# Kernel tuning notes

Measured on AMD Instinct MI355X. Metric: run time of the kernel, lower is better.

The kernel has to match this reference:

```python
import jax, jax.numpy as jnp
import numpy as np

H = 32        # query heads
KVH = 8       # key/value heads (GQA)
D = 160       # head_dim = 5120 / 32
ROT = 40      # rotary_ndims = head_dim * partial_rotary_factor (0.25)
THETA = 10000.0
NEG = -1e30


def setup_inputs() -> dict:
    key = jax.random.key(0)
    k0, k1, k2, k3 = jax.random.split(key, 4)
    B, S, E = 1, 2048, 5120
    QKV_OUT = H * D + 2 * KVH * D  # 7680
    hidden_states = jax.random.normal(k0, (B, S, E), jnp.float32)
    w_qkv = jax.random.normal(k1, (QKV_OUT, E), jnp.float32) * 0.02
    b_qkv = jax.random.normal(k2, (QKV_OUT,), jnp.float32) * 0.02
    w_o = jax.random.normal(k3, (E, E), jnp.float32) * 0.02
    positions = jnp.arange(S, dtype=jnp.int32)
    return {"hidden_states": hidden_states, "positions": positions,
            "w_qkv": w_qkv, "b_qkv": b_qkv, "w_o": w_o}


def _partial_rope(x, cos, sin):
    # x: [B,S,h,D]; neox-style rotation on first ROT dims, pass-through rest
    rot, rest = x[..., :ROT], x[..., ROT:]
    x1, x2 = jnp.split(rot, 2, axis=-1)
    rotated = jnp.concatenate([x1 * cos - x2 * sin, x2 * cos + x1 * sin], axis=-1)
    return jnp.concatenate([rotated, rest], axis=-1)


def reference(hidden_states, positions, w_qkv, b_qkv, w_o):
    B, S, E = hidden_states.shape
    qkv = jnp.einsum('bse,oe->bso', hidden_states, w_qkv) + b_qkv
    q = qkv[..., :H * D].reshape(B, S, H, D)
    k = qkv[..., H * D:H * D + KVH * D].reshape(B, S, KVH, D)
    v = qkv[..., H * D + KVH * D:].reshape(B, S, KVH, D)

    # partial rotary embedding
    inv_freq = 1.0 / (THETA ** (jnp.arange(0, ROT, 2, dtype=jnp.float32) / ROT))
    freqs = positions.astype(jnp.float32)[:, None] * inv_freq  # [S, ROT/2]
    cos = jnp.cos(freqs)[None, :, None, :]
    sin = jnp.sin(freqs)[None, :, None, :]
    q = _partial_rope(q, cos, sin)
    k = _partial_rope(k, cos, sin)

    # grouped-query causal attention (prefill path of PagedAttention)
    G = H // KVH
    qg = q.reshape(B, S, KVH, G, D)
    scores = jnp.einsum('bqkgd,bskd->bkgqs', qg, k) * (D ** -0.5)
    causal = jnp.tril(jnp.ones((S, S), bool))
    scores = jnp.where(causal, scores, NEG)
    attn = jax.nn.softmax(scores, axis=-1)
    out = jnp.einsum('bkgqs,bskd->bqkgd', attn, v).reshape(B, S, H * D)
    return jnp.einsum('bsf,ef->bse', out, w_o)
```

## Files before the change

### kernel.cpp

```cpp
#include <hip/hip_runtime.h>

typedef __attribute__((ext_vector_type(8))) short short8;
typedef __attribute__((ext_vector_type(4))) float f32x4;
typedef __attribute__((ext_vector_type(16))) float f32x16;
typedef __attribute__((ext_vector_type(4))) unsigned short ushort4v;
typedef __attribute__((ext_vector_type(4))) unsigned u32x4;

#define S_LEN 2048
#define E_DIM 5120
#define NH 32
#define NKVH 8
#define HD 160
#define QKV_OUT (NH*HD + 2*NKVH*HD)
#define NPAIR 20
#define ROT_D 40

__device__ __forceinline__ unsigned short f2b(float f) {
  unsigned u = __builtin_bit_cast(unsigned, f);
  u += 0x7fffu + ((u >> 16) & 1u);
  return (unsigned short)(u >> 16);
}
__device__ __forceinline__ float b2f(unsigned short b) {
  return __builtin_bit_cast(float, ((unsigned)b) << 16);
}

typedef const __attribute__((address_space(1))) unsigned gu32;
typedef __attribute__((address_space(3))) unsigned lu32;
__device__ __forceinline__ void gll16(const void* g, void* l) {
  __builtin_amdgcn_global_load_lds((gu32*)g, (lu32*)l, 16, 0, 0);
}
#define MFMA16(a, b, c) __builtin_amdgcn_mfma_f32_16x16x32_bf16(a, b, c, 0, 0, 0)
#define MFMA32(a, b, c) __builtin_amdgcn_mfma_f32_32x32x16_bf16(a, b, c, 0, 0, 0)
#define SBAR() asm volatile("s_barrier" ::: "memory")

__global__ __launch_bounds__(256) void f32_to_bf16_vec(const float* __restrict__ in,
                                                       unsigned short* __restrict__ out,
                                                       long n4) {
  long i = (long)blockIdx.x * blockDim.x + threadIdx.x;
  long stride = (long)gridDim.x * blockDim.x;
  for (; i < n4; i += stride) {
    float4 v = ((const float4*)in)[i];
    ushort4v o = { f2b(v.x), f2b(v.y), f2b(v.z), f2b(v.w) };
    ((ushort4v*)out)[i] = o;
  }
}

__global__ __launch_bounds__(256) void build_trig(const int* __restrict__ positions,
                                                  float* __restrict__ cosT,
                                                  float* __restrict__ sinT) {
  int idx = blockIdx.x * blockDim.x + threadIdx.x;
  if (idx >= S_LEN * NPAIR) return;
  int s = idx / NPAIR, i = idx - s * NPAIR;
  float inv = powf(10000.0f, -(float)i / (float)NPAIR);
  float f = (float)positions[s] * inv;
  cosT[idx] = cosf(f);
  sinT[idx] = sinf(f);
}

template <bool BIAS, bool OUT_BF16>
__global__ __launch_bounds__(512, 2) void gemm8(const unsigned short* __restrict__ A,
                                                const unsigned short* __restrict__ B,
                                                const float* __restrict__ bias,
                                                void* __restrict__ Cp,
                                                int N) {
  constexpr int K = E_DIM;
  constexpr int NT = K / 64;
  int bid = blockIdx.x;
  int bm = bid & 7, bn = bid >> 3;
  int tid = threadIdx.x;
  int w = tid >> 6, l = tid & 63;
  int g = l >> 4, c = l & 15;
  int wm = w >> 2, wn = w & 3;

  __shared__ __align__(16) unsigned short LA[2][2][8192];
  __shared__ __align__(16) unsigned short LB[2][2][8192];

  f32x4 acc[8][4];
#pragma unroll
  for (int i = 0; i < 8; ++i)
#pragma unroll
    for (int j = 0; j < 4; ++j) acc[i][j] = f32x4{0.f, 0.f, 0.f, 0.f};

  int uU[2] = {tid, 512 + tid};
  const unsigned short* Ag[2];
  const unsigned short* Bg[2];
#pragma unroll
  for (int j = 0; j < 2; ++j) {
    int u = uU[j];
    int wmG = u >> 9, rlA = (u >> 3) & 63, sl = u & 7;
    Ag[j] = A + (size_t)(bm * 256 + wmG * 128 + rlA) * K + (sl ^ (rlA & 7)) * 8;
    int wnG = u >> 8, rlB = (u >> 3) & 31;
    Bg[j] = B + (size_t)(bn * 256 + wnG * 64 + rlB) * K + (sl ^ (rlB & 7)) * 8;
  }

  auto stageA = [&](int t, int rg, int db) {
#pragma unroll
    for (int j = 0; j < 2; ++j)
      gll16(Ag[j] + (size_t)rg * 64 * K + t * 64, (char*)&LA[db][rg][0] + uU[j] * 16);
  };
  auto stageB = [&](int t, int cg, int db) {
#pragma unroll
    for (int j = 0; j < 2; ++j)
      gll16(Bg[j] + (size_t)cg * 32 * K + t * 64, (char*)&LB[db][cg][0] + uU[j] * 16);
  };

  int aA = wm * 4096 + c * 64;
  int bB = wn * 2048 + c * 64;
  int s0 = (g ^ (c & 7)) * 8;
  int s1 = ((4 + g) ^ (c & 7)) * 8;

  short8 a[8], b0[4], b1[4];

  stageA(0, 0, 0); stageB(0, 0, 0); stageB(0, 1, 0); stageA(0, 1, 0);
  stageA(1, 0, 1); stageB(1, 0, 1); stageB(1, 1, 1);
  asm volatile("s_waitcnt vmcnt(6)" ::: "memory");
  SBAR();

  for (int t = 0; t < NT; ++t) {
    int db = t & 1;
    const unsigned short* la0 = &LA[db][0][0];
    const unsigned short* la1 = &LA[db][1][0];
    const unsigned short* lb0 = &LB[db][0][0];
    const unsigned short* lb1 = &LB[db][1][0];
    bool tail = (t >= NT - 3);

#pragma unroll
    for (int fm = 0; fm < 4; ++fm) {
      a[2 * fm + 0] = *(const short8*)&la0[aA + fm * 1024 + s0];
      a[2 * fm + 1] = *(const short8*)&la0[aA + fm * 1024 + s1];
    }
#pragma unroll
    for (int fn = 0; fn < 2; ++fn) {
      b0[2 * fn + 0] = *(const short8*)&lb0[bB + fn * 1024 + s0];
      b0[2 * fn + 1] = *(const short8*)&lb0[bB + fn * 1024 + s1];
    }
    if (t + 1 < NT) stageA(t + 1, 1, db ^ 1);
    SBAR();
    __builtin_amdgcn_s_setprio(1);
#pragma unroll
    for (int fm = 0; fm < 4; ++fm)
#pragma unroll
      for (int fn = 0; fn < 2; ++fn) {
        acc[fm][fn] = MFMA16(a[2 * fm + 0], b0[2 * fn + 0], acc[fm][fn]);
        acc[fm][fn] = MFMA16(a[2 * fm + 1], b0[2 * fn + 1], acc[fm][fn]);
      }
    __builtin_amdgcn_s_setprio(0);
    SBAR();

#pragma unroll
    for (int fn = 0; fn < 2; ++fn) {
      b1[2 * fn + 0] = *(const short8*)&lb1[bB + fn * 1024 + s0];
      b1[2 * fn + 1] = *(const short8*)&lb1[bB + fn * 1024 + s1];
    }
    if (t + 2 < NT) stageA(t + 2, 0, db);
    SBAR();
    __builtin_amdgcn_s_setprio(1);
#pragma unroll
    for (int fm = 0; fm < 4; ++fm)
#pragma unroll
      for (int fn = 0; fn < 2; ++fn) {
        acc[fm][fn + 2] = MFMA16(a[2 * fm + 0], b1[2 * fn + 0], acc[fm][fn + 2]);
        acc[fm][fn + 2] = MFMA16(a[2 * fm + 1], b1[2 * fn + 1], acc[fm][fn + 2]);
      }
    __builtin_amdgcn_s_setprio(0);
    if (tail)
      asm volatile("s_waitcnt vmcnt(0)" ::: "memory");
    else
      asm volatile("s_waitcnt vmcnt(10)" ::: "memory");
    SBAR();

#pragma unroll
    for (int fm = 0; fm < 4; ++fm) {
      a[2 * fm + 0] = *(const short8*)&la1[aA + fm * 1024 + s0];
      a[2 * fm + 1] = *(const short8*)&la1[aA + fm * 1024 + s1];
    }
    if (t + 2 < NT) stageB(t + 2, 0, db);
    SBAR();
    __builtin_amdgcn_s_setprio(1);
#pragma unroll
    for (int fm = 0; fm < 4; ++fm)
#pragma unroll
      for (int fn = 0; fn < 2; ++fn) {
        acc[fm + 4][fn + 2] = MFMA16(a[2 * fm + 0], b1[2 * fn + 0], acc[fm + 4][fn + 2]);
        acc[fm + 4][fn + 2] = MFMA16(a[2 * fm + 1], b1[2 * fn + 1], acc[fm + 4][fn + 2]);
      }
    __builtin_amdgcn_s_setprio(0);
    SBAR();

    if (t + 2 < NT) stageB(t + 2, 1, db);
    SBAR();
    __builtin_amdgcn_s_setprio(1);
#pragma unroll
    for (int fm = 0; fm < 4; ++fm)
#pragma unroll
      for (int fn = 0; fn < 2; ++fn) {
        acc[fm + 4][fn] = MFMA16(a[2 * fm + 0], b0[2 * fn + 0], acc[fm + 4][fn]);
        acc[fm + 4][fn] = MFMA16(a[2 * fm + 1], b0[2 * fn + 1], acc[fm + 4][fn]);
      }
    __builtin_amdgcn_s_setprio(0);
    if (tail)
      asm volatile("s_waitcnt vmcnt(0)" ::: "memory");
    else
      asm volatile("s_waitcnt vmcnt(8)" ::: "memory");
    SBAR();
  }

#pragma unroll
  for (int FN = 0; FN < 4; ++FN) {
    int n = bn * 256 + wn * 64 + (FN >> 1) * 32 + (FN & 1) * 16 + c;
    float bv = BIAS ? bias[n] : 0.f;
#pragma unroll
    for (int FM = 0; FM < 8; ++FM) {
#pragma unroll
      for (int r = 0; r < 4; ++r) {
        int m = bm * 256 + wm * 128 + (FM >> 2) * 64 + (FM & 3) * 16 + 4 * g + r;
        float v = acc[FM][FN][r] + bv;
        if (OUT_BF16)
          ((unsigned short*)Cp)[(size_t)m * N + n] = f2b(v);
        else
          ((float*)Cp)[(size_t)m * N + n] = v;
      }
    }
  }
}

__global__ __launch_bounds__(256) void rope_qk(const unsigned short* __restrict__ qkv,
                                               const float* __restrict__ cosT,
                                               const float* __restrict__ sinT,
                                               unsigned short* __restrict__ Q,
                                               unsigned short* __restrict__ K) {
  int s = blockIdx.x;
  int tid = threadIdx.x;
  const unsigned short* row = qkv + (size_t)s * QKV_OUT;
  const float* cs = cosT + s * NPAIR;
  const float* sn = sinT + s * NPAIR;
  for (int p = tid; p < 40 * NPAIR; p += 256) {
    int head = p / NPAIR, i = p - head * NPAIR;
    float x1 = b2f(row[head * HD + i]);
    float x2 = b2f(row[head * HD + i + NPAIR]);
    float o1 = x1 * cs[i] - x2 * sn[i];
    float o2 = x2 * cs[i] + x1 * sn[i];
    unsigned short* dst = (head < NH) ? (Q + ((size_t)head * S_LEN + s) * HD)
                                      : (K + ((size_t)(head - NH) * S_LEN + s) * HD);
    dst[i] = f2b(o1);
    dst[i + NPAIR] = f2b(o2);
  }
  for (int u = tid; u < 40 * 15; u += 256) {
    int head = u / 15;
    int d8 = ROT_D + (u - head * 15) * 8;
    short8 v = *(const short8*)(row + head * HD + d8);
    unsigned short* dst = (head < NH) ? (Q + ((size_t)head * S_LEN + s) * HD)
                                      : (K + ((size_t)(head - NH) * S_LEN + s) * HD);
    *(short8*)(dst + d8) = v;
  }
}

__global__ __launch_bounds__(256) void v_transpose(const unsigned short* __restrict__ qkv,
                                                   unsigned short* __restrict__ Vt) {
  int st = blockIdx.x;
  int kvh = blockIdx.y;
  int tid = threadIdx.x;
  __shared__ __align__(16) unsigned short T[64][168];
  const unsigned short* src = qkv + (size_t)(st * 64) * QKV_OUT + NH * HD + NKVH * HD + kvh * HD;
#pragma unroll
  for (int i = 0; i < 5; ++i) {
    int u = tid + i * 256;
    int r = u / 20, sl = u - r * 20;
    int4 val = *(const int4*)(src + (size_t)r * QKV_OUT + sl * 8);
    *(int4*)((char*)&T[r][0] + sl * 16) = val;
  }
  __syncthreads();
  unsigned short* dst = Vt + (size_t)kvh * HD * S_LEN + st * 64;
#pragma unroll
  for (int i = 0; i < 5; ++i) {
    int u = tid + i * 256;
    int d = u >> 3, sc = u & 7;
    unsigned short tmp[8];
#pragma unroll
    for (int j = 0; j < 8; ++j) tmp[j] = T[sc * 8 + j][d];
    *(int4*)(dst + (size_t)d * S_LEN + sc * 8) = *(const int4*)tmp;
  }
}

__global__ __launch_bounds__(256, 1) void attn_kernel(const unsigned short* __restrict__ Q,
                                                      const unsigned short* __restrict__ K,
                                                      const unsigned short* __restrict__ Vt,
                                                      unsigned short* __restrict__ Ao) {
  int bid = blockIdx.x;
  int kvh = bid & 7;
  int sidx = bid >> 3;
  int strip = (sidx < 32) ? (63 - sidx) : (sidx - 32);
  int nt = strip + 1;
  int qbase = strip * 32;
  int tid = threadIdx.x;
  int w = tid >> 6, l = tid & 63;
  int lo5 = l & 31, hi = l >> 5;
  int h = kvh * 4 + w;

  __shared__ __align__(16) unsigned short KL[2][10 * 512];
  __shared__ __align__(16) unsigned short VL[2][10 * 512];

  const unsigned short* kg = K + (size_t)kvh * S_LEN * HD;
  const unsigned short* vg = Vt + (size_t)kvh * HD * S_LEN;
  const unsigned short* qg = Q + ((size_t)h * S_LEN + qbase + lo5) * HD;

  short8 qf[10];
#pragma unroll
  for (int f = 0; f < 10; ++f) qf[f] = *(const short8*)(qg + f * 16 + hi * 8);

  auto STAGE = [&](int t, int buf) {
#pragma unroll
    for (int i = 0; i < 5; ++i) {
      int cc = w * 5 + i;
      if (cc < 10) {
        gll16(kg + ((size_t)(t * 32) + lo5) * HD + cc * 16 + hi * 8,
              (void*)&KL[buf][cc * 512]);
      } else {
        int m = cc - 10;
        int dblk = m >> 1, half = m & 1;
        gll16(vg + (size_t)(dblk * 32 + lo5) * S_LEN + t * 32 + half * 16 + hi * 8,
              (void*)&VL[buf][m * 512]);
      }
    }
  };

  const float sm_scale = 0.07905694150420949f;
  f32x16 acc[5];
#pragma unroll
  for (int d = 0; d < 5; ++d)
#pragma unroll
    for (int r = 0; r < 16; ++r) acc[d][r] = 0.f;
  float l_run = 0.f;

  STAGE(0, 0);
  if (nt > 1) STAGE(1, 1);

#pragma unroll 1
  for (int t = 0; t < nt; ++t) {
    int buf = t & 1;
    if (t + 1 < nt)
      asm volatile("s_waitcnt vmcnt(5)" ::: "memory");
    else
      asm volatile("s_waitcnt vmcnt(0)" ::: "memory");
    SBAR();

    f32x16 S;
#pragma unroll
    for (int r = 0; r < 16; ++r) S[r] = 0.f;
    __builtin_amdgcn_s_setprio(1);
#pragma unroll
    for (int f = 0; f < 10; ++f) {
      short8 kf = *(const short8*)&KL[buf][f * 512 + l * 8];
      S = MFMA32(kf, qf[f], S);
    }
    __builtin_amdgcn_s_setprio(0);

    float e[16];
    float rsum = 0.f;
    if (t == nt - 1) {
#pragma unroll
      for (int r = 0; r < 16; ++r) {
        int kvloc = (r & 3) + 8 * (r >> 2) + 4 * hi;
        float x = (kvloc <= lo5) ? S[r] * sm_scale : -1e30f;
        e[r] = __expf(x);
        rsum += e[r];
      }
    } else {
#pragma unroll
      for (int r = 0; r < 16; ++r) {
        e[r] = __expf(S[r] * sm_scale);
        rsum += e[r];
      }
    }
    rsum += __shfl_xor(rsum, 32);
    l_run += rsum;

    unsigned xp[8];
#pragma unroll
    for (int i = 0; i < 8; ++i)
      asm("v_cvt_pk_bf16_f32 %0, %1, %2" : "=v"(xp[i]) : "v"(e[2 * i]), "v"(e[2 * i + 1]));
    asm volatile("v_permlane32_swap_b32 %0, %1" : "+v"(xp[0]), "+v"(xp[2]));
    asm volatile("v_permlane32_swap_b32 %0, %1" : "+v"(xp[1]), "+v"(xp[3]));
    asm volatile("v_permlane32_swap_b32 %0, %1" : "+v"(xp[4]), "+v"(xp[6]));
    asm volatile("v_permlane32_swap_b32 %0, %1" : "+v"(xp[5]), "+v"(xp[7]));
    u32x4 w0 = {xp[0], xp[1], xp[2], xp[3]};
    u32x4 w1 = {xp[4], xp[5], xp[6], xp[7]};
    short8 pa0 = __builtin_bit_cast(short8, w0);
    short8 pa1 = __builtin_bit_cast(short8, w1);

    __builtin_amdgcn_s_setprio(1);
#pragma unroll
    for (int dblk = 0; dblk < 5; ++dblk) {
      short8 v0 = *(const short8*)&VL[buf][(2 * dblk + 0) * 512 + l * 8];
      short8 v1 = *(const short8*)&VL[buf][(2 * dblk + 1) * 512 + l * 8];
      acc[dblk] = MFMA32(pa0, v0, acc[dblk]);
      acc[dblk] = MFMA32(pa1, v1, acc[dblk]);
    }
    __builtin_amdgcn_s_setprio(0);
    SBAR();
    if (t + 2 < nt) STAGE(t + 2, buf);
  }

  float rinv = 1.f / l_run;
  float ri[16];
#pragma unroll
  for (int r = 0; r < 16; ++r) ri[r] = __shfl(rinv, (r & 3) + 8 * (r >> 2) + 4 * hi);
#pragma unroll
  for (int dblk = 0; dblk < 5; ++dblk)
#pragma unroll
    for (int r = 0; r < 16; ++r) {
      int q = (r & 3) + 8 * (r >> 2) + 4 * hi;
      Ao[(size_t)(qbase + q) * E_DIM + h * HD + dblk * 32 + lo5] = f2b(acc[dblk][r] * ri[r]);
    }
}

extern "C" void kernel_launch(void* const* d_in, const int* in_sizes, int n_in,
                              void* d_out, int out_size, void* d_ws, size_t ws_size,
                              hipStream_t stream) {
  const float* hidden = (const float*)d_in[0];
  const int* positions = (const int*)d_in[1];
  const float* w_qkv = (const float*)d_in[2];
  const float* b_qkv = (const float*)d_in[3];
  const float* w_o = (const float*)d_in[4];
  float* out = (float*)d_out;

  char* ws = (char*)d_ws;
  size_t off = 0;
  auto alloc = [&](size_t bytes) {
    void* p = ws + off;
    off += (bytes + 255) & ~(size_t)255;
    return p;
  };
  unsigned short* hB = (unsigned short*)alloc((size_t)S_LEN * E_DIM * 2);
  unsigned short* wqkvB = (unsigned short*)alloc((size_t)QKV_OUT * E_DIM * 2);
  unsigned short* woB = (unsigned short*)alloc((size_t)E_DIM * E_DIM * 2);
  unsigned short* qkvB = (unsigned short*)alloc((size_t)S_LEN * QKV_OUT * 2);
  unsigned short* Qb = (unsigned short*)alloc((size_t)NH * S_LEN * HD * 2);
  unsigned short* Kb = (unsigned short*)alloc((size_t)NKVH * S_LEN * HD * 2);
  unsigned short* Vtb = (unsigned short*)alloc((size_t)NKVH * HD * S_LEN * 2);
  float* cosT = (float*)alloc((size_t)S_LEN * NPAIR * 4);
  float* sinT = (float*)alloc((size_t)S_LEN * NPAIR * 4);
  if (off > ws_size) return;

  unsigned short* Ao = hB;

  f32_to_bf16_vec<<<2048, 256, 0, stream>>>(hidden, hB, (long)S_LEN * E_DIM / 4);
  f32_to_bf16_vec<<<2048, 256, 0, stream>>>(w_qkv, wqkvB, (long)QKV_OUT * E_DIM / 4);
  f32_to_bf16_vec<<<2048, 256, 0, stream>>>(w_o, woB, (long)E_DIM * E_DIM / 4);
  build_trig<<<(S_LEN * NPAIR + 255) / 256, 256, 0, stream>>>(positions, cosT, sinT);

  gemm8<true, true><<<dim3((QKV_OUT / 256) * 8), 512, 0, stream>>>(
      hB, wqkvB, b_qkv, qkvB, QKV_OUT);

  rope_qk<<<S_LEN, 256, 0, stream>>>(qkvB, cosT, sinT, Qb, Kb);
  v_transpose<<<dim3(S_LEN / 64, NKVH), 256, 0, stream>>>(qkvB, Vtb);

  attn_kernel<<<dim3(512), 256, 0, stream>>>(Qb, Kb, Vtb, Ao);

  gemm8<false, false><<<dim3((E_DIM / 256) * 8), 512, 0, stream>>>(
      Ao, woB, nullptr, out, E_DIM);
}
```

Before: 489.2 us.

## Fuse fp32-to-bf16 weight conversion into GEMM B-operand staging

Removes the separate conversion kernels for w_qkv and w_o. The GEMM now loads fp32 weight tiles into registers, packs them to bf16 with v_cvt_pk_bf16_f32 and writes them to LDS, restructuring the pipeline's wait counts and stage placement. This avoids an extra full read and write of both weight matrices, but the GEMM reads twice as many B bytes and spends VALU and register work on conversion inside the main loop. The epilogue row/column indexing is also changed to match a new fragment mapping.

```diff
diff --git a/kernel.cpp b/kernel.cpp
--- a/kernel.cpp
+++ b/kernel.cpp
@@ -59,7 +59,7 @@
 
 template <bool BIAS, bool OUT_BF16>
 __global__ __launch_bounds__(512, 2) void gemm8(const unsigned short* __restrict__ A,
-                                                const unsigned short* __restrict__ B,
+                                                const float* __restrict__ Bf32,
                                                 const float* __restrict__ bias,
                                                 void* __restrict__ Cp,
                                                 int N) {
@@ -83,25 +83,54 @@
 
   int uU[2] = {tid, 512 + tid};
   const unsigned short* Ag[2];
-  const unsigned short* Bg[2];
 #pragma unroll
   for (int j = 0; j < 2; ++j) {
     int u = uU[j];
     int wmG = u >> 9, rlA = (u >> 3) & 63, sl = u & 7;
     Ag[j] = A + (size_t)(bm * 256 + wmG * 128 + rlA) * K + (sl ^ (rlA & 7)) * 8;
-    int wnG = u >> 8, rlB = (u >> 3) & 31;
-    Bg[j] = B + (size_t)(bn * 256 + wnG * 64 + rlB) * K + (sl ^ (rlB & 7)) * 8;
-  }
-
+  }
   auto stageA = [&](int t, int rg, int db) {
 #pragma unroll
     for (int j = 0; j < 2; ++j)
       gll16(Ag[j] + (size_t)rg * 64 * K + t * 64, (char*)&LA[db][rg][0] + uU[j] * 16);
   };
-  auto stageB = [&](int t, int cg, int db) {
-#pragma unroll
-    for (int j = 0; j < 2; ++j)
-      gll16(Bg[j] + (size_t)cg * 32 * K + t * 64, (char*)&LB[db][cg][0] + uU[j] * 16);
+
+  const float* Bpj[2];
+  int wofB[2];
+#pragma unroll
+  for (int j = 0; j < 2; ++j) {
+    int r = w * 16 + j * 8 + (l >> 3);
+    int sg = ((l & 7) ^ (r & 7)) * 8;
+    wofB[j] = (r * 8 + (l & 7)) * 16;
+    int rowg = (r >> 5) * 64 + (r & 31);
+    Bpj[j] = Bf32 + (size_t)(bn * 256 + rowg) * K + sg;
+  }
+  const size_t cgstep = (size_t)32 * K;
+
+  float4 bst[2][2][2];
+  auto issueB = [&](int t) {
+#pragma unroll
+    for (int cg = 0; cg < 2; ++cg)
+#pragma unroll
+      for (int j = 0; j < 2; ++j) {
+        const float* p = Bpj[j] + cg * cgstep + (size_t)t * 64;
+        bst[cg][j][0] = *(const float4*)p;
+        bst[cg][j][1] = *(const float4*)(p + 4);
+      }
+  };
+  auto writeB = [&](int db) {
+#pragma unroll
+    for (int cg = 0; cg < 2; ++cg)
+#pragma unroll
+      for (int j = 0; j < 2; ++j) {
+        unsigned w0, w1, w2, w3;
+        asm("v_cvt_pk_bf16_f32 %0, %1, %2" : "=v"(w0) : "v"(bst[cg][j][0].x), "v"(bst[cg][j][0].y));
+        asm("v_cvt_pk_bf16_f32 %0, %1, %2" : "=v"(w1) : "v"(bst[cg][j][0].z), "v"(bst[cg][j][0].w));
+        asm("v_cvt_pk_bf16_f32 %0, %1, %2" : "=v"(w2) : "v"(bst[cg][j][1].x), "v"(bst[cg][j][1].y));
+        asm("v_cvt_pk_bf16_f32 %0, %1, %2" : "=v"(w3) : "v"(bst[cg][j][1].z), "v"(bst[cg][j][1].w));
+        u32x4 pk = {w0, w1, w2, w3};
+        *(u32x4*)((char*)&LB[db][cg][0] + wofB[j]) = pk;
+      }
   };
 
   int aA = wm * 4096 + c * 64;
@@ -111,9 +140,15 @@
 
   short8 a[8], b0[4], b1[4];
 
-  stageA(0, 0, 0); stageB(0, 0, 0); stageB(0, 1, 0); stageA(0, 1, 0);
-  stageA(1, 0, 1); stageB(1, 0, 1); stageB(1, 1, 1);
-  asm volatile("s_waitcnt vmcnt(6)" ::: "memory");
+  issueB(0);
+  stageA(0, 0, 0); stageA(0, 1, 0);
+  stageA(1, 0, 1); stageA(1, 1, 1);
+  asm volatile("s_waitcnt vmcnt(8)" ::: "memory");
+  writeB(0);
+  issueB(1);
+  asm volatile("s_waitcnt vmcnt(0)" ::: "memory");
+  writeB(1);
+  asm volatile("s_waitcnt lgkmcnt(0)" ::: "memory");
   SBAR();
 
   for (int t = 0; t < NT; ++t) {
@@ -122,7 +157,7 @@
     const unsigned short* la1 = &LA[db][1][0];
     const unsigned short* lb0 = &LB[db][0][0];
     const unsigned short* lb1 = &LB[db][1][0];
-    bool tail = (t >= NT - 3);
+    bool have2 = (t + 2 < NT);
 
 #pragma unroll
     for (int fm = 0; fm < 4; ++fm) {
@@ -134,7 +169,7 @@
       b0[2 * fn + 0] = *(const short8*)&lb0[bB + fn * 1024 + s0];
       b0[2 * fn + 1] = *(const short8*)&lb0[bB + fn * 1024 + s1];
     }
-    if (t + 1 < NT) stageA(t + 1, 1, db ^ 1);
+    if (have2) issueB(t + 2);
     SBAR();
     __builtin_amdgcn_s_setprio(1);
 #pragma unroll
@@ -152,7 +187,7 @@
       b1[2 * fn + 0] = *(const short8*)&lb1[bB + fn * 1024 + s0];
       b1[2 * fn + 1] = *(const short8*)&lb1[bB + fn * 1024 + s1];
     }
-    if (t + 2 < NT) stageA(t + 2, 0, db);
+    if (have2) stageA(t + 2, 0, db);
     SBAR();
     __builtin_amdgcn_s_setprio(1);
 #pragma unroll
@@ -163,10 +198,6 @@
         acc[fm][fn + 2] = MFMA16(a[2 * fm + 1], b1[2 * fn + 1], acc[fm][fn + 2]);
       }
     __builtin_amdgcn_s_setprio(0);
-    if (tail)
-      asm volatile("s_waitcnt vmcnt(0)" ::: "memory");
-    else
-      asm volatile("s_waitcnt vmcnt(10)" ::: "memory");
     SBAR();
 
 #pragma unroll
@@ -174,7 +205,12 @@
       a[2 * fm + 0] = *(const short8*)&la1[aA + fm * 1024 + s0];
       a[2 * fm + 1] = *(const short8*)&la1[aA + fm * 1024 + s1];
     }
-    if (t + 2 < NT) stageB(t + 2, 0, db);
+    if (have2) {
+      asm volatile("s_waitcnt vmcnt(2)" ::: "memory");
+      writeB(db);
+    } else {
+      asm volatile("s_waitcnt vmcnt(0)" ::: "memory");
+    }
     SBAR();
     __builtin_amdgcn_s_setprio(1);
 #pragma unroll
@@ -185,10 +221,10 @@
         acc[fm + 4][fn + 2] = MFMA16(a[2 * fm + 1], b1[2 * fn + 1], acc[fm + 4][fn + 2]);
       }
     __builtin_amdgcn_s_setprio(0);
-    SBAR();
-
-    if (t + 2 < NT) stageB(t + 2, 1, db);
-    SBAR();
+    asm volatile("s_waitcnt lgkmcnt(0)" ::: "memory");
+    SBAR();
+
+    if (have2) stageA(t + 2, 1, db);
     __builtin_amdgcn_s_setprio(1);
 #pragma unroll
     for (int fm = 0; fm < 4; ++fm)
@@ -198,23 +234,19 @@
         acc[fm + 4][fn] = MFMA16(a[2 * fm + 1], b0[2 * fn + 1], acc[fm + 4][fn]);
       }
     __builtin_amdgcn_s_setprio(0);
-    if (tail)
-      asm volatile("s_waitcnt vmcnt(0)" ::: "memory");
-    else
-      asm volatile("s_waitcnt vmcnt(8)" ::: "memory");
-    SBAR();
-  }
-
-#pragma unroll
-  for (int FN = 0; FN < 4; ++FN) {
-    int n = bn * 256 + wn * 64 + (FN >> 1) * 32 + (FN & 1) * 16 + c;
+    SBAR();
+  }
+
+#pragma unroll
+  for (int fn = 0; fn < 4; ++fn) {
+    int n = bn * 256 + wn * 64 + fn * 16 + c;
     float bv = BIAS ? bias[n] : 0.f;
 #pragma unroll
-    for (int FM = 0; FM < 8; ++FM) {
+    for (int fm = 0; fm < 8; ++fm) {
 #pragma unroll
       for (int r = 0; r < 4; ++r) {
-        int m = bm * 256 + wm * 128 + (FM >> 2) * 64 + (FM & 3) * 16 + 4 * g + r;
-        float v = acc[FM][FN][r] + bv;
+        int m = bm * 256 + wm * 128 + fm * 16 + 4 * g + r;
+        float v = acc[fm][fn][r] + bv;
         if (OUT_BF16)
           ((unsigned short*)Cp)[(size_t)m * N + n] = f2b(v);
         else
@@ -432,8 +464,6 @@
     return p;
   };
   unsigned short* hB = (unsigned short*)alloc((size_t)S_LEN * E_DIM * 2);
-  unsigned short* wqkvB = (unsigned short*)alloc((size_t)QKV_OUT * E_DIM * 2);
-  unsigned short* woB = (unsigned short*)alloc((size_t)E_DIM * E_DIM * 2);
   unsigned short* qkvB = (unsigned short*)alloc((size_t)S_LEN * QKV_OUT * 2);
   unsigned short* Qb = (unsigned short*)alloc((size_t)NH * S_LEN * HD * 2);
   unsigned short* Kb = (unsigned short*)alloc((size_t)NKVH * S_LEN * HD * 2);
@@ -445,12 +475,10 @@
   unsigned short* Ao = hB;
 
   f32_to_bf16_vec<<<2048, 256, 0, stream>>>(hidden, hB, (long)S_LEN * E_DIM / 4);
-  f32_to_bf16_vec<<<2048, 256, 0, stream>>>(w_qkv, wqkvB, (long)QKV_OUT * E_DIM / 4);
-  f32_to_bf16_vec<<<2048, 256, 0, stream>>>(w_o, woB, (long)E_DIM * E_DIM / 4);
   build_trig<<<(S_LEN * NPAIR + 255) / 256, 256, 0, stream>>>(positions, cosT, sinT);
 
   gemm8<true, true><<<dim3((QKV_OUT / 256) * 8), 512, 0, stream>>>(
-      hB, wqkvB, b_qkv, qkvB, QKV_OUT);
+      hB, w_qkv, b_qkv, qkvB, QKV_OUT);
 
   rope_qk<<<S_LEN, 256, 0, stream>>>(qkvB, cosT, sinT, Qb, Kb);
   v_transpose<<<dim3(S_LEN / 64, NKVH), 256, 0, stream>>>(qkvB, Vtb);
@@ -458,5 +486,5 @@
   attn_kernel<<<dim3(512), 256, 0, stream>>>(Qb, Kb, Vtb, Ao);
 
   gemm8<false, false><<<dim3((E_DIM / 256) * 8), 512, 0, stream>>>(
-      Ao, woB, nullptr, out, E_DIM);
-}
+      Ao, w_o, nullptr, out, E_DIM);
+}
```

Result: slower. 641.2 us (+31.1%).

## Add 256x160-tile output-projection GEMM to fill all CUs; drop one barrier

Applied to the files above, without the earlier changes.

Adds a specialized gemm160 kernel for the output projection. It uses 256x160 tiles, so the grid has 256 blocks instead of 160, aiming to occupy every CU on the device and reduce wave-quantization idle time. Its B-operand staging is split into three chunks spread across the k-loop phases, with per-wave vmcnt waits. The QKV GEMM also loses one workgroup barrier before its second MFMA phase, and its epilogue index arithmetic is simplified to an equivalent form. The per-wave waitcnt schedule and the removed barrier add race risk if the counts or ordering are wrong.

```diff
diff --git a/kernel.cpp b/kernel.cpp
--- a/kernel.cpp
+++ b/kernel.cpp
@@ -188,7 +188,6 @@
     SBAR();
 
     if (t + 2 < NT) stageB(t + 2, 1, db);
-    SBAR();
     __builtin_amdgcn_s_setprio(1);
 #pragma unroll
     for (int fm = 0; fm < 4; ++fm)
@@ -207,18 +206,175 @@
 
 #pragma unroll
   for (int FN = 0; FN < 4; ++FN) {
-    int n = bn * 256 + wn * 64 + (FN >> 1) * 32 + (FN & 1) * 16 + c;
+    int n = bn * 256 + wn * 64 + FN * 16 + c;
     float bv = BIAS ? bias[n] : 0.f;
 #pragma unroll
     for (int FM = 0; FM < 8; ++FM) {
 #pragma unroll
       for (int r = 0; r < 4; ++r) {
-        int m = bm * 256 + wm * 128 + (FM >> 2) * 64 + (FM & 3) * 16 + 4 * g + r;
+        int m = bm * 256 + wm * 128 + FM * 16 + 4 * g + r;
         float v = acc[FM][FN][r] + bv;
         if (OUT_BF16)
           ((unsigned short*)Cp)[(size_t)m * N + n] = f2b(v);
         else
           ((float*)Cp)[(size_t)m * N + n] = v;
+      }
+    }
+  }
+}
+
+__global__ __launch_bounds__(512, 2) void gemm160(const unsigned short* __restrict__ A,
+                                                  const unsigned short* __restrict__ B,
+                                                  float* __restrict__ C) {
+  constexpr int K = E_DIM;
+  constexpr int NT = K / 64;
+  int bid = blockIdx.x;
+  int bm = bid & 7, bn = bid >> 3;
+  int tid = threadIdx.x;
+  int w = tid >> 6, l = tid & 63;
+  int g = l >> 4, c = l & 15;
+  int wm = w >> 1, wn = w & 1;
+
+  __shared__ __align__(16) unsigned short LA[2][2][8192];
+  __shared__ __align__(16) unsigned short LB[2][20 * 512];
+
+  f32x4 acc[4][5];
+#pragma unroll
+  for (int i = 0; i < 4; ++i)
+#pragma unroll
+    for (int j = 0; j < 5; ++j) acc[i][j] = f32x4{0.f, 0.f, 0.f, 0.f};
+
+  int uU[2] = {tid, 512 + tid};
+  const unsigned short* Ag[2];
+#pragma unroll
+  for (int j = 0; j < 2; ++j) {
+    int u = uU[j];
+    int wmG = u >> 9, rlA = (u >> 3) & 63, sl = u & 7;
+    Ag[j] = A + (size_t)(bm * 256 + wmG * 128 + rlA) * K + (sl ^ (rlA & 7)) * 8;
+  }
+  auto stageA = [&](int t, int rg, int db) {
+#pragma unroll
+    for (int j = 0; j < 2; ++j)
+      gll16(Ag[j] + (size_t)rg * 64 * K + t * 64, (char*)&LA[db][rg][0] + uU[j] * 16);
+  };
+
+  int rowin = l >> 3, slb = l & 7;
+  int swz = (slb ^ rowin) * 8;
+  int chN01 = (w < 4) ? w : 6 + w;
+  int chN23 = (w < 4) ? 4 + w : 10 + w;
+  int chN4 = (w < 2) ? 8 + w : 16 + w;
+  const unsigned short* srcN01 = B + (size_t)(bn * 160 + chN01 * 8 + rowin) * K + swz;
+  const unsigned short* srcN23 = B + (size_t)(bn * 160 + chN23 * 8 + rowin) * K + swz;
+  const unsigned short* srcN4 = B + (size_t)(bn * 160 + ((w < 4) ? chN4 * 8 : 0) + rowin) * K + swz;
+  auto stB = [&](const unsigned short* src, int ch, int t, int db) {
+    gll16(src + t * 64, (char*)&LB[db][0] + ch * 1024 + l * 16);
+  };
+
+  int rgA = wm & 1;
+  int aA = ((wm >> 1) * 64 + c) * 64;
+  int bB = (wn * 80 + c) * 64;
+  int s0 = (g ^ (c & 7)) * 8;
+  int s1 = ((4 + g) ^ (c & 7)) * 8;
+
+  short8 a[8], b01[4], b23[4], bn4[2];
+
+  stageA(0, 0, 0); stageA(0, 1, 0);
+  stB(srcN01, chN01, 0, 0); stB(srcN23, chN23, 0, 0);
+  if (w < 4) stB(srcN4, chN4, 0, 0);
+  stageA(1, 0, 1); stageA(1, 1, 1);
+  stB(srcN01, chN01, 1, 1); stB(srcN23, chN23, 1, 1);
+  asm volatile("s_waitcnt vmcnt(0)" ::: "memory");
+  SBAR();
+
+  for (int t = 0; t < NT; ++t) {
+    int db = t & 1;
+    const unsigned short* la = &LA[db][rgA][0];
+    const unsigned short* lb = &LB[db][0];
+    bool tail = (t >= NT - 2);
+
+#pragma unroll
+    for (int fm = 0; fm < 4; ++fm) {
+      a[2 * fm + 0] = *(const short8*)&la[aA + fm * 1024 + s0];
+      a[2 * fm + 1] = *(const short8*)&la[aA + fm * 1024 + s1];
+    }
+#pragma unroll
+    for (int fn = 0; fn < 2; ++fn) {
+      b01[2 * fn + 0] = *(const short8*)&lb[bB + fn * 1024 + s0];
+      b01[2 * fn + 1] = *(const short8*)&lb[bB + fn * 1024 + s1];
+    }
+    if (t + 1 < NT && w < 4) stB(srcN4, chN4, t + 1, db ^ 1);
+    SBAR();
+    __builtin_amdgcn_s_setprio(1);
+#pragma unroll
+    for (int fm = 0; fm < 4; ++fm)
+#pragma unroll
+      for (int fn = 0; fn < 2; ++fn) {
+        acc[fm][fn] = MFMA16(a[2 * fm + 0], b01[2 * fn + 0], acc[fm][fn]);
+        acc[fm][fn] = MFMA16(a[2 * fm + 1], b01[2 * fn + 1], acc[fm][fn]);
+      }
+    __builtin_amdgcn_s_setprio(0);
+    if (tail)
+      asm volatile("s_waitcnt vmcnt(0)" ::: "memory");
+    else if (w < 4)
+      asm volatile("s_waitcnt vmcnt(8)" ::: "memory");
+    else
+      asm volatile("s_waitcnt vmcnt(6)" ::: "memory");
+    SBAR();
+
+#pragma unroll
+    for (int fn = 0; fn < 2; ++fn) {
+      b23[2 * fn + 0] = *(const short8*)&lb[bB + (2 + fn) * 1024 + s0];
+      b23[2 * fn + 1] = *(const short8*)&lb[bB + (2 + fn) * 1024 + s1];
+    }
+    if (t + 2 < NT) {
+      stageA(t + 2, 0, db); stageA(t + 2, 1, db);
+      stB(srcN01, chN01, t + 2, db);
+    }
+    SBAR();
+    __builtin_amdgcn_s_setprio(1);
+#pragma unroll
+    for (int fm = 0; fm < 4; ++fm)
+#pragma unroll
+      for (int fn = 0; fn < 2; ++fn) {
+        acc[fm][fn + 2] = MFMA16(a[2 * fm + 0], b23[2 * fn + 0], acc[fm][fn + 2]);
+        acc[fm][fn + 2] = MFMA16(a[2 * fm + 1], b23[2 * fn + 1], acc[fm][fn + 2]);
+      }
+    __builtin_amdgcn_s_setprio(0);
+    if (tail)
+      asm volatile("s_waitcnt vmcnt(0)" ::: "memory");
+    else if (w < 4)
+      asm volatile("s_waitcnt vmcnt(12)" ::: "memory");
+    SBAR();
+
+    bn4[0] = *(const short8*)&lb[bB + 4 * 1024 + s0];
+    bn4[1] = *(const short8*)&lb[bB + 4 * 1024 + s1];
+    if (t + 2 < NT) stB(srcN23, chN23, t + 2, db);
+    SBAR();
+    __builtin_amdgcn_s_setprio(1);
+#pragma unroll
+    for (int fm = 0; fm < 4; ++fm) {
+      acc[fm][4] = MFMA16(a[2 * fm + 0], bn4[0], acc[fm][4]);
+      acc[fm][4] = MFMA16(a[2 * fm + 1], bn4[1], acc[fm][4]);
+    }
+    __builtin_amdgcn_s_setprio(0);
+    if (tail)
+      asm volatile("s_waitcnt vmcnt(0)" ::: "memory");
+    else if (w < 4)
+      asm volatile("s_waitcnt vmcnt(8)" ::: "memory");
+    else
+      asm volatile("s_waitcnt vmcnt(7)" ::: "memory");
+    SBAR();
+  }
+
+#pragma unroll
+  for (int fn = 0; fn < 5; ++fn) {
+    int n = bn * 160 + wn * 80 + fn * 16 + c;
+#pragma unroll
+    for (int fm = 0; fm < 4; ++fm) {
+#pragma unroll
+      for (int r = 0; r < 4; ++r) {
+        int m = bm * 256 + wm * 64 + fm * 16 + 4 * g + r;
+        C[(size_t)m * E_DIM + n] = acc[fm][fn][r];
       }
     }
   }
@@ -457,6 +613,5 @@
 
   attn_kernel<<<dim3(512), 256, 0, stream>>>(Qb, Kb, Vtb, Ao);
 
-  gemm8<false, false><<<dim3((E_DIM / 256) * 8), 512, 0, stream>>>(
-      Ao, woB, nullptr, out, E_DIM);
-}
+  gemm160<<<dim3(256), 512, 0, stream>>>(Ao, woB, out);
+}
```

Result: no change. 485.7 us (-0.7%).
